# Optimization experiments

Hardware: AMD Instinct MI355X
Metric: run time of the kernel (lower is better)

The kernel has to match this reference:

```python
import jax, jax.numpy as jnp
import numpy as np

NUM_STEPS = 5  # matches init num_steps
N_NODES = 500_000
N_EDGES = 32_000_000


def setup_inputs() -> dict:
    key = jax.random.key(0)
    k1, k2, k3 = jax.random.split(key, 3)
    prior_probs = jax.random.uniform(k1, (N_NODES,), dtype=jnp.float32)
    edge_index = jax.random.randint(k2, (2, N_EDGES), 0, N_NODES, dtype=jnp.int32)
    edge_probs = jax.random.uniform(k3, (N_EDGES,), dtype=jnp.float32)
    return {"prior_probs": prior_probs, "edge_index": edge_index, "edge_probs": edge_probs}


def reference(prior_probs, edge_index, edge_probs):
    num_nodes = prior_probs.shape[0]
    source = edge_index[0]
    target = edge_index[1]
    p_t_u = prior_probs
    prod_terms = jnp.ones_like(prior_probs)
    for _ in range(NUM_STEPS):
        # gather node activation at source, weight by edge prob, scatter-add into target
        message = edge_probs * p_t_u[source]            # [E]
        agg = jax.ops.segment_sum(message, target, num_segments=num_nodes)  # [N]
        delta = 1.0 - jnp.exp(-agg)
        new_p_t_u = prod_terms * delta
        prod_terms = prod_terms * (1.0 - new_p_t_u)
        p_t_u = new_p_t_u
    p_final = 1.0 - prod_terms + prior_probs
    return p_final.reshape(-1, 1)
```

## Files before the change

### kernel.cpp

```cpp
#include <hip/hip_runtime.h>
#include <hip/hip_fp16.h>

#define NUM_STEPS 5
typedef unsigned int u32;

#define RSH 10
#define RSZ 1024
#define SB  512
#define HT  512
#define ST  512
#define NBMAX 512
#define BINS 8
#define SPLIT 2
#define SRC_BITS 19
#define SRC_MASK 0x7FFFFu

static inline size_t align256(size_t x){ return (x + 255) & ~(size_t)255; }


__global__ void init_fast(const float* __restrict__ prior, __half* __restrict__ p,
                          float* __restrict__ prod, int n){
    int i = blockIdx.x*blockDim.x + threadIdx.x;
    if(i<n){ p[i]=__float2half_rn(prior[i]); prod[i]=1.0f; }
}

__global__ void hist_kernel(const int* __restrict__ dst, long long E, int B,
                            u32* __restrict__ blk_cnt){
    extern __shared__ u32 hist[];
    int sb = blockIdx.x;
    long long E4 = E >> 2;
    long long chunk = (E4 + SB - 1)/SB;
    long long i0 = (long long)sb*chunk;
    long long i1 = i0 + chunk; if(i1 > E4) i1 = E4;
    for(int b=threadIdx.x; b<B; b+=blockDim.x) hist[b]=0;
    __syncthreads();
    const int4* d4 = (const int4*)dst;
    for(long long i=i0+threadIdx.x; i<i1; i+=blockDim.x){
        int4 d = d4[i];
        atomicAdd(&hist[((u32)d.x)>>RSH], 1u);
        atomicAdd(&hist[((u32)d.y)>>RSH], 1u);
        atomicAdd(&hist[((u32)d.z)>>RSH], 1u);
        atomicAdd(&hist[((u32)d.w)>>RSH], 1u);
    }
    if(sb==0){
        for(long long e=(E4<<2)+threadIdx.x; e<E; e+=blockDim.x)
            atomicAdd(&hist[((u32)dst[e])>>RSH], 1u);
    }
    __syncthreads();
    for(int b=threadIdx.x; b<B; b+=blockDim.x) blk_cnt[(size_t)sb*B + b] = hist[b];
}

__global__ void colscan_kernel(u32* __restrict__ blk_cnt, int B, u32* __restrict__ tot){
    __shared__ u32 s[SB];
    int b = blockIdx.x, t = threadIdx.x;
    u32 v = blk_cnt[(size_t)t*B + b];
    s[t] = v; __syncthreads();
    for(int off=1; off<SB; off<<=1){
        u32 x = (t>=off) ? s[t-off] : 0;
        __syncthreads();
        s[t] += x;
        __syncthreads();
    }
    blk_cnt[(size_t)t*B + b] = s[t] - v;
    if(t==SB-1) tot[b] = s[SB-1];
}

__global__ void basescan_kernel(const u32* __restrict__ tot, u32* __restrict__ base, int B){
    __shared__ u32 s[256];
    int t = threadIdx.x;
    u32 v0 = (2*t   < B) ? tot[2*t]   : 0;
    u32 v1 = (2*t+1 < B) ? tot[2*t+1] : 0;
    u32 sum = v0 + v1;
    s[t] = sum; __syncthreads();
    for(int off=1; off<256; off<<=1){
        u32 x = (t>=off) ? s[t-off] : 0;
        __syncthreads();
        s[t] += x;
        __syncthreads();
    }
    u32 run = s[t] - sum;
    if(2*t   < B) base[2*t]   = run;
    if(2*t+1 < B) base[2*t+1] = run + v0;
    if(t==255) base[B] = s[255];
}

__global__ __launch_bounds__(ST) void
scatter_kernel(const int* __restrict__ src, const int* __restrict__ dst,
               const float* __restrict__ ep, long long E, int B,
               const u32* __restrict__ blk_rel, const u32* __restrict__ base,
               uint2* __restrict__ edges){
    __shared__ uint2 bin[NBMAX][BINS];
    __shared__ u32 cnt[NBMAX];
    __shared__ u32 gcur[NBMAX];
    const int sb = blockIdx.x, t = threadIdx.x;
    long long E4 = E >> 2;
    long long chunk = (E4 + SB - 1)/SB;
    long long i0 = (long long)sb*chunk;
    long long i1 = i0 + chunk; if(i1 > E4) i1 = E4;
    for(int b=t; b<B; b+=ST){ cnt[b]=0; gcur[b]=base[b]+blk_rel[(size_t)sb*B+b]; }
    __syncthreads();
    const int4*   s4=(const int4*)src;
    const int4*   d4=(const int4*)dst;
    const float4* w4=(const float4*)ep;
    for(long long it=i0; it<i1; it+=ST){
        long long i = it + t;
        bool valid = (i < i1);
        u32 bk[4]; u32 sl[4]; uint2 pl[4];
        if(valid){
            int4 s=s4[i]; int4 d=d4[i]; float4 w=w4[i];
            u32 dd;
            dd=(u32)d.x; bk[0]=dd>>RSH; pl[0]=make_uint2(((u32)s.x)|((dd&(RSZ-1))<<SRC_BITS), __float_as_uint(w.x));
            dd=(u32)d.y; bk[1]=dd>>RSH; pl[1]=make_uint2(((u32)s.y)|((dd&(RSZ-1))<<SRC_BITS), __float_as_uint(w.y));
            dd=(u32)d.z; bk[2]=dd>>RSH; pl[2]=make_uint2(((u32)s.z)|((dd&(RSZ-1))<<SRC_BITS), __float_as_uint(w.z));
            dd=(u32)d.w; bk[3]=dd>>RSH; pl[3]=make_uint2(((u32)s.w)|((dd&(RSZ-1))<<SRC_BITS), __float_as_uint(w.w));
            #pragma unroll
            for(int k=0;k<4;k++) sl[k]=atomicAdd(&cnt[bk[k]],1u);
        }
        __syncthreads();
        if(valid){
            #pragma unroll
            for(int k=0;k<4;k++){
                if(sl[k] < BINS) bin[bk[k]][sl[k]] = pl[k];
                else             edges[gcur[bk[k]] + sl[k]] = pl[k];
            }
        }
        __syncthreads();
        for(int b=t; b<B; b+=ST){
            u32 c = cnt[b];
            if(c >= BINS){
                u32 g = gcur[b];
                #pragma unroll
                for(int k2=0;k2<BINS;k2++) edges[g+k2] = bin[b][k2];
                gcur[b] = g + c;
                cnt[b]  = 0;
            }
        }
        __syncthreads();
    }
    if(sb==0){
        long long tb = E4<<2;
        int nt = (int)(E - tb);
        if(nt > 0){
            bool v = (t < nt);
            u32 bk0=0, sl0=0; uint2 pl0=make_uint2(0,0);
            if(v){
                u32 dd=(u32)dst[tb+t]; bk0=dd>>RSH;
                pl0=make_uint2(((u32)src[tb+t])|((dd&(RSZ-1))<<SRC_BITS), __float_as_uint(ep[tb+t]));
                sl0=atomicAdd(&cnt[bk0],1u);
            }
            __syncthreads();
            if(v){ if(sl0<BINS) bin[bk0][sl0]=pl0; else edges[gcur[bk0]+sl0]=pl0; }
            __syncthreads();
        }
    }
    for(int b=t; b<B; b+=ST){
        u32 c = cnt[b]; if(c > BINS) c = BINS;
        u32 g = gcur[b];
        for(u32 k2=0;k2<c;k2++) edges[g+k2] = bin[b][k2];
    }
}

__global__ __launch_bounds__(512) void
step_kernel(const uint2* __restrict__ edges, const u32* __restrict__ base,
            const __half* __restrict__ p, float* __restrict__ pacc){
    __shared__ float acc[2][RSZ];
    int blk = blockIdx.x;
    int b   = blk >> 1;
    int part= blk & 1;
    int t   = threadIdx.x;
    for(int k=t; k<RSZ; k+=512){ acc[0][k]=0.0f; acc[1][k]=0.0f; }
    __syncthreads();
    u32 e0 = base[b], e1 = base[b+1];
    u32 cnt = e1 - e0;
    u32 s0 = e0 + (cnt*(u32)part)/SPLIT;
    u32 s1 = e0 + (cnt*(u32)(part+1))/SPLIT;
    int rep = t & 1;
    u32 n = s1 - s0;
    u32 m = n >> 11;
    u32 eb = s0 + t;
    for(u32 it=0; it<m; ++it){
        uint2 a0 = edges[eb];
        uint2 a1 = edges[eb+512];
        uint2 a2 = edges[eb+1024];
        uint2 a3 = edges[eb+1536];
        float p0 = __half2float(p[a0.x & SRC_MASK]);
        float p1 = __half2float(p[a1.x & SRC_MASK]);
        float p2 = __half2float(p[a2.x & SRC_MASK]);
        float p3 = __half2float(p[a3.x & SRC_MASK]);
        atomicAdd(&acc[rep][a0.x >> SRC_BITS], __uint_as_float(a0.y)*p0);
        atomicAdd(&acc[rep][a1.x >> SRC_BITS], __uint_as_float(a1.y)*p1);
        atomicAdd(&acc[rep][a2.x >> SRC_BITS], __uint_as_float(a2.y)*p2);
        atomicAdd(&acc[rep][a3.x >> SRC_BITS], __uint_as_float(a3.y)*p3);
        eb += 2048;
    }
    for(u32 e=eb; e<s1; e+=512){
        uint2 a = edges[e];
        atomicAdd(&acc[rep][a.x >> SRC_BITS],
                  __uint_as_float(a.y)*__half2float(p[a.x & SRC_MASK]));
    }
    __syncthreads();
    float* dstp = pacc + (size_t)blk * RSZ;
    for(int k=t; k<RSZ; k+=512) dstp[k] = acc[0][k] + acc[1][k];
}

__global__ void combine_kernel(const float* __restrict__ pacc, __half* __restrict__ p,
                               float* __restrict__ prod, const float* __restrict__ prior,
                               float* __restrict__ out, int n, int final_step){
    int i = blockIdx.x*blockDim.x + threadIdx.x;
    if(i < n){
        int b = i >> RSH, k = i & (RSZ-1);
        float a = pacc[(size_t)(b*SPLIT    )*RSZ + k]
                + pacc[(size_t)(b*SPLIT + 1)*RSZ + k];
        float pr_old = prod[i];
        float np = pr_old * (1.0f - expf(-a));
        float pr = pr_old * (1.0f - np);
        prod[i] = pr;
        p[i] = __float2half_rn(np);
        if(final_step) out[i] = 1.0f - pr + prior[i];
    }
}


__global__ void init_kernel(const float* __restrict__ prior, float* __restrict__ p,
                            float* __restrict__ prod, float* __restrict__ agg, int n){
    int i = blockIdx.x*blockDim.x + threadIdx.x;
    if(i<n){ p[i]=prior[i]; prod[i]=1.0f; agg[i]=0.0f; }
}

__global__ void edge_kernel(const int* __restrict__ src, const int* __restrict__ dst,
                            const float* __restrict__ ep, const float* __restrict__ p,
                            float* __restrict__ agg, int e4, int e_rem, long long e4base){
    int i = blockIdx.x*blockDim.x + threadIdx.x;
    if(i < e4){
        int4   s = ((const int4*)src)[i];
        int4   t = ((const int4*)dst)[i];
        float4 w = ((const float4*)ep)[i];
        atomicAdd(&agg[t.x], w.x * p[s.x]);
        atomicAdd(&agg[t.y], w.y * p[s.y]);
        atomicAdd(&agg[t.z], w.z * p[s.z]);
        atomicAdd(&agg[t.w], w.w * p[s.w]);
    }
    if(blockIdx.x==0 && threadIdx.x < e_rem){
        long long e = e4base + threadIdx.x;
        atomicAdd(&agg[dst[e]], ep[e]*p[src[e]]);
    }
}

__global__ void node_kernel(float* __restrict__ p, float* __restrict__ prod,
                            float* __restrict__ agg, const float* __restrict__ prior,
                            float* __restrict__ out, int n, int final_step){
    int i = blockIdx.x*blockDim.x + threadIdx.x;
    if(i<n){
        float a = agg[i]; agg[i]=0.0f;
        float pr_old = prod[i];
        float np = pr_old*(1.0f - expf(-a));
        float pr = pr_old*(1.0f - np);
        prod[i]=pr; p[i]=np;
        if(final_step) out[i] = 1.0f - pr + prior[i];
    }
}


extern "C" void kernel_launch(void* const* d_in, const int* in_sizes, int n_in,
                              void* d_out, int out_size, void* d_ws, size_t ws_size,
                              hipStream_t stream){
    const float* prior = (const float*)d_in[0];
    const int*   eidx  = (const int*)d_in[1];
    const float* ep    = (const float*)d_in[2];

    const int n = in_sizes[0];
    const long long E = (long long)in_sizes[2];
    const int* src = eidx;
    const int* dst = eidx + E;
    float* out = (float*)d_out;

    const int B = (n + RSZ - 1) >> RSH;

    size_t szNh  = align256((size_t)n * 2);
    size_t szN   = align256((size_t)n * 4);
    size_t szB1  = align256((size_t)(B + 1) * 4);
    size_t szB   = align256((size_t)B * 4);
    size_t szCnt = align256((size_t)SB * B * 4);
    size_t szAcc = align256((size_t)SPLIT * B * RSZ * 4);
    size_t szE2  = align256((size_t)E * 8);

    size_t off_p    = 0;
    size_t off_prod = off_p + szNh;
    size_t off_base = off_prod + szN;
    size_t off_tot  = off_base + szB1;
    size_t off_cnt  = off_tot + szB;
    size_t off_acc  = off_cnt + szCnt;
    size_t off_edge = off_acc + szAcc;
    size_t need     = off_edge + szE2;

    char* ws = (char*)d_ws;

    if(ws_size >= need && n < (1 << SRC_BITS) && B <= NBMAX){
        __half* p    = (__half*)(ws + off_p);
        float*  prod = (float*) (ws + off_prod);
        u32*    base = (u32*)   (ws + off_base);
        u32*    tot  = (u32*)   (ws + off_tot);
        u32*    cnt  = (u32*)   (ws + off_cnt);
        float*  pacc = (float*) (ws + off_acc);
        uint2*  edges= (uint2*) (ws + off_edge);

        const int nb_n = (n + 255)/256;
        init_fast<<<nb_n, 256, 0, stream>>>(prior, p, prod, n);
        hist_kernel<<<SB, HT, (size_t)B*4, stream>>>(dst, E, B, cnt);
        colscan_kernel<<<B, SB, 0, stream>>>(cnt, B, tot);
        basescan_kernel<<<1, 256, 0, stream>>>(tot, base, B);
        scatter_kernel<<<SB, ST, 0, stream>>>(src, dst, ep, E, B, cnt, base, edges);

        for(int step=0; step<NUM_STEPS; ++step){
            step_kernel<<<B*SPLIT, 512, 0, stream>>>(edges, base, p, pacc);
            combine_kernel<<<nb_n, 256, 0, stream>>>(pacc, p, prod, prior, out, n,
                                                     step == NUM_STEPS-1 ? 1 : 0);
        }
    } else {
        float* p    = (float*)d_ws;
        float* prod = p + n;
        float* agg  = prod + n;
        const int nb_n = (n + 255)/256;
        init_kernel<<<nb_n, 256, 0, stream>>>(prior, p, prod, agg, n);
        const int e4 = (int)(E/4);
        const int e_rem = (int)(E%4);
        const long long e4base = (long long)e4*4;
        const int nb_e = (e4 + 255)/256;
        for(int step=0; step<NUM_STEPS; ++step){
            edge_kernel<<<nb_e, 256, 0, stream>>>(src, dst, ep, p, agg, e4, e_rem, e4base);
            node_kernel<<<nb_n, 256, 0, stream>>>(p, prod, agg, prior, out, n,
                                                  step == NUM_STEPS-1 ? 1 : 0);
        }
    }
}
```

Before: 1.162 ms.

## Sub-sort edges by source within each destination bucket for gather locality

Adds a per-bucket counting sort that reorders the packed edges by the high bits of the source index into a second edge buffer. The step kernel then reads the sorted buffer, so its gathers of p[source] touch nearby addresses, which should cut scattered memory traffic across the five steps. SB also doubles to 1024 histogram/scatter blocks, and colscan gets a matching launch bound. The cost is one extra pass over all edges and a second E-sized workspace buffer; when the workspace is too small, the sort is skipped.

New measurement: 1.601 ms. 1.38x slower.

```diff
diff --git a/kernel.cpp b/kernel.cpp
--- a/kernel.cpp
+++ b/kernel.cpp
@@ -6,7 +6,7 @@
 
 #define RSH 10
 #define RSZ 1024
-#define SB  512
+#define SB  1024
 #define HT  512
 #define ST  512
 #define NBMAX 512
@@ -14,6 +14,8 @@
 #define SPLIT 2
 #define SRC_BITS 19
 #define SRC_MASK 0x7FFFFu
+#define SBIN 256
+#define SBIN_SH 11
 
 static inline size_t align256(size_t x){ return (x + 255) & ~(size_t)255; }
 
@@ -50,7 +52,8 @@
     for(int b=threadIdx.x; b<B; b+=blockDim.x) blk_cnt[(size_t)sb*B + b] = hist[b];
 }
 
-__global__ void colscan_kernel(u32* __restrict__ blk_cnt, int B, u32* __restrict__ tot){
+__global__ __launch_bounds__(SB) void
+colscan_kernel(u32* __restrict__ blk_cnt, int B, u32* __restrict__ tot){
     __shared__ u32 s[SB];
     int b = blockIdx.x, t = threadIdx.x;
     u32 v = blk_cnt[(size_t)t*B + b];
@@ -157,6 +160,37 @@
         u32 c = cnt[b]; if(c > BINS) c = BINS;
         u32 g = gcur[b];
         for(u32 k2=0;k2<c;k2++) edges[g+k2] = bin[b][k2];
+    }
+}
+
+__global__ __launch_bounds__(512) void
+srcsort_kernel(const uint2* __restrict__ in, const u32* __restrict__ base,
+               uint2* __restrict__ outb){
+    __shared__ u32 hist[SBIN];
+    __shared__ u32 scn[SBIN];
+    __shared__ u32 cur[SBIN];
+    int b = blockIdx.x, t = threadIdx.x;
+    u32 e0 = base[b], e1 = base[b+1];
+    if(t < SBIN) hist[t] = 0;
+    __syncthreads();
+    for(u32 e=e0+t; e<e1; e+=512)
+        atomicAdd(&hist[(in[e].x & SRC_MASK) >> SBIN_SH], 1u);
+    __syncthreads();
+    if(t < SBIN) scn[t] = hist[t];
+    __syncthreads();
+    for(int off=1; off<SBIN; off<<=1){
+        u32 x = 0;
+        if(t < SBIN && t >= off) x = scn[t-off];
+        __syncthreads();
+        if(t < SBIN) scn[t] += x;
+        __syncthreads();
+    }
+    if(t < SBIN) cur[t] = e0 + scn[t] - hist[t];
+    __syncthreads();
+    for(u32 e=e0+t; e<e1; e+=512){
+        uint2 pk = in[e];
+        u32 pos = atomicAdd(&cur[(pk.x & SRC_MASK) >> SBIN_SH], 1u);
+        outb[pos] = pk;
     }
 }
 
@@ -291,11 +325,13 @@
     size_t off_cnt  = off_tot + szB;
     size_t off_acc  = off_cnt + szCnt;
     size_t off_edge = off_acc + szAcc;
-    size_t need     = off_edge + szE2;
+    size_t need_ns  = off_edge + szE2;
+    size_t off_edg2 = need_ns;
+    size_t need_full= off_edg2 + szE2;
 
     char* ws = (char*)d_ws;
 
-    if(ws_size >= need && n < (1 << SRC_BITS) && B <= NBMAX){
+    if(ws_size >= need_ns && n < (1 << SRC_BITS) && B <= NBMAX){
         __half* p    = (__half*)(ws + off_p);
         float*  prod = (float*) (ws + off_prod);
         u32*    base = (u32*)   (ws + off_base);
@@ -303,6 +339,8 @@
         u32*    cnt  = (u32*)   (ws + off_cnt);
         float*  pacc = (float*) (ws + off_acc);
         uint2*  edges= (uint2*) (ws + off_edge);
+        uint2*  edg2 = (uint2*) (ws + off_edg2);
+        const bool do_sort = (ws_size >= need_full);
 
         const int nb_n = (n + 255)/256;
         init_fast<<<nb_n, 256, 0, stream>>>(prior, p, prod, n);
@@ -311,8 +349,14 @@
         basescan_kernel<<<1, 256, 0, stream>>>(tot, base, B);
         scatter_kernel<<<SB, ST, 0, stream>>>(src, dst, ep, E, B, cnt, base, edges);
 
+        const uint2* step_edges = edges;
+        if(do_sort){
+            srcsort_kernel<<<B, 512, 0, stream>>>(edges, base, edg2);
+            step_edges = edg2;
+        }
+
         for(int step=0; step<NUM_STEPS; ++step){
-            step_kernel<<<B*SPLIT, 512, 0, stream>>>(edges, base, p, pacc);
+            step_kernel<<<B*SPLIT, 512, 0, stream>>>(step_edges, base, p, pacc);
             combine_kernel<<<nb_n, 256, 0, stream>>>(pacc, p, prod, prior, out, n,
                                                      step == NUM_STEPS-1 ? 1 : 0);
         }
```

## Fuse all propagation steps into one cooperative kernel with grid sync

Applied to the files above, without the earlier changes.

Replaces the per-step step_kernel plus combine_kernel pairs, and the init kernel, with a single cooperative launch. Each block owns one 1024-node bucket, keeps the node's product term in a register and accumulates in shared memory, and uses grid.sync between phases. This removes the global partial-accumulator round trip and repeated launches, but loses the SPLIT=2 edge partitioning and the 4-way unrolled loads. The histogram scatter block count (SB) is also doubled. It relies on all B (~489) blocks of 1024 threads being co-resident for cooperative launch.

Result: slower. 3.599 ms (+209.7%).

```diff
diff --git a/kernel.cpp b/kernel.cpp
--- a/kernel.cpp
+++ b/kernel.cpp
@@ -1,28 +1,24 @@
 #include <hip/hip_runtime.h>
 #include <hip/hip_fp16.h>
+#include <hip/hip_cooperative_groups.h>
+
+namespace cg = cooperative_groups;
 
 #define NUM_STEPS 5
 typedef unsigned int u32;
 
 #define RSH 10
 #define RSZ 1024
-#define SB  512
+#define SB  1024
 #define HT  512
 #define ST  512
 #define NBMAX 512
 #define BINS 8
-#define SPLIT 2
 #define SRC_BITS 19
 #define SRC_MASK 0x7FFFFu
 
 static inline size_t align256(size_t x){ return (x + 255) & ~(size_t)255; }
 
-
-__global__ void init_fast(const float* __restrict__ prior, __half* __restrict__ p,
-                          float* __restrict__ prod, int n){
-    int i = blockIdx.x*blockDim.x + threadIdx.x;
-    if(i<n){ p[i]=__float2half_rn(prior[i]); prod[i]=1.0f; }
-}
 
 __global__ void hist_kernel(const int* __restrict__ dst, long long E, int B,
                             u32* __restrict__ blk_cnt){
@@ -50,7 +46,8 @@
     for(int b=threadIdx.x; b<B; b+=blockDim.x) blk_cnt[(size_t)sb*B + b] = hist[b];
 }
 
-__global__ void colscan_kernel(u32* __restrict__ blk_cnt, int B, u32* __restrict__ tot){
+__global__ __launch_bounds__(SB) void
+colscan_kernel(u32* __restrict__ blk_cnt, int B, u32* __restrict__ tot){
     __shared__ u32 s[SB];
     int b = blockIdx.x, t = threadIdx.x;
     u32 v = blk_cnt[(size_t)t*B + b];
@@ -160,64 +157,38 @@
     }
 }
 
-__global__ __launch_bounds__(512) void
-step_kernel(const uint2* __restrict__ edges, const u32* __restrict__ base,
-            const __half* __restrict__ p, float* __restrict__ pacc){
+__global__ __launch_bounds__(1024, 2) void
+fused_steps(const uint2* __restrict__ edges, const u32* __restrict__ base,
+            __half* __restrict__ p, const float* __restrict__ prior,
+            float* __restrict__ out, int n){
+    cg::grid_group grid = cg::this_grid();
     __shared__ float acc[2][RSZ];
-    int blk = blockIdx.x;
-    int b   = blk >> 1;
-    int part= blk & 1;
-    int t   = threadIdx.x;
-    for(int k=t; k<RSZ; k+=512){ acc[0][k]=0.0f; acc[1][k]=0.0f; }
-    __syncthreads();
-    u32 e0 = base[b], e1 = base[b+1];
-    u32 cnt = e1 - e0;
-    u32 s0 = e0 + (cnt*(u32)part)/SPLIT;
-    u32 s1 = e0 + (cnt*(u32)(part+1))/SPLIT;
-    int rep = t & 1;
-    u32 n = s1 - s0;
-    u32 m = n >> 11;
-    u32 eb = s0 + t;
-    for(u32 it=0; it<m; ++it){
-        uint2 a0 = edges[eb];
-        uint2 a1 = edges[eb+512];
-        uint2 a2 = edges[eb+1024];
-        uint2 a3 = edges[eb+1536];
-        float p0 = __half2float(p[a0.x & SRC_MASK]);
-        float p1 = __half2float(p[a1.x & SRC_MASK]);
-        float p2 = __half2float(p[a2.x & SRC_MASK]);
-        float p3 = __half2float(p[a3.x & SRC_MASK]);
-        atomicAdd(&acc[rep][a0.x >> SRC_BITS], __uint_as_float(a0.y)*p0);
-        atomicAdd(&acc[rep][a1.x >> SRC_BITS], __uint_as_float(a1.y)*p1);
-        atomicAdd(&acc[rep][a2.x >> SRC_BITS], __uint_as_float(a2.y)*p2);
-        atomicAdd(&acc[rep][a3.x >> SRC_BITS], __uint_as_float(a3.y)*p3);
-        eb += 2048;
-    }
-    for(u32 e=eb; e<s1; e+=512){
-        uint2 a = edges[e];
-        atomicAdd(&acc[rep][a.x >> SRC_BITS],
-                  __uint_as_float(a.y)*__half2float(p[a.x & SRC_MASK]));
-    }
-    __syncthreads();
-    float* dstp = pacc + (size_t)blk * RSZ;
-    for(int k=t; k<RSZ; k+=512) dstp[k] = acc[0][k] + acc[1][k];
-}
-
-__global__ void combine_kernel(const float* __restrict__ pacc, __half* __restrict__ p,
-                               float* __restrict__ prod, const float* __restrict__ prior,
-                               float* __restrict__ out, int n, int final_step){
-    int i = blockIdx.x*blockDim.x + threadIdx.x;
-    if(i < n){
-        int b = i >> RSH, k = i & (RSZ-1);
-        float a = pacc[(size_t)(b*SPLIT    )*RSZ + k]
-                + pacc[(size_t)(b*SPLIT + 1)*RSZ + k];
-        float pr_old = prod[i];
-        float np = pr_old * (1.0f - expf(-a));
-        float pr = pr_old * (1.0f - np);
-        prod[i] = pr;
-        p[i] = __float2half_rn(np);
-        if(final_step) out[i] = 1.0f - pr + prior[i];
-    }
+    const int b = blockIdx.x, t = threadIdx.x;
+    const int i = (b << RSH) + t;
+    acc[0][t] = 0.0f; acc[1][t] = 0.0f;
+    if(i < n) p[i] = __float2half_rn(prior[i]);
+    float prodr = 1.0f;
+    const u32 e0 = base[b], e1 = base[b+1];
+    const int rep = t & 1;
+    __threadfence();
+    grid.sync();
+    for(int step=0; step<NUM_STEPS; ++step){
+        for(u32 e = e0 + t; e < e1; e += 1024){
+            uint2 pk = edges[e];
+            atomicAdd(&acc[rep][pk.x >> SRC_BITS],
+                      __uint_as_float(pk.y) * __half2float(p[pk.x & SRC_MASK]));
+        }
+        __threadfence();
+        grid.sync();
+        float a = acc[0][t] + acc[1][t];
+        acc[0][t] = 0.0f; acc[1][t] = 0.0f;
+        float np = prodr * (1.0f - expf(-a));
+        prodr *= (1.0f - np);
+        if(i < n) p[i] = __float2half_rn(np);
+        __threadfence();
+        grid.sync();
+    }
+    if(i < n) out[i] = 1.0f - prodr + prior[i];
 }
 
 
@@ -277,45 +248,37 @@
     const int B = (n + RSZ - 1) >> RSH;
 
     size_t szNh  = align256((size_t)n * 2);
-    size_t szN   = align256((size_t)n * 4);
     size_t szB1  = align256((size_t)(B + 1) * 4);
     size_t szB   = align256((size_t)B * 4);
     size_t szCnt = align256((size_t)SB * B * 4);
-    size_t szAcc = align256((size_t)SPLIT * B * RSZ * 4);
     size_t szE2  = align256((size_t)E * 8);
 
     size_t off_p    = 0;
-    size_t off_prod = off_p + szNh;
-    size_t off_base = off_prod + szN;
+    size_t off_base = off_p + szNh;
     size_t off_tot  = off_base + szB1;
     size_t off_cnt  = off_tot + szB;
-    size_t off_acc  = off_cnt + szCnt;
-    size_t off_edge = off_acc + szAcc;
+    size_t off_edge = off_cnt + szCnt;
     size_t need     = off_edge + szE2;
 
     char* ws = (char*)d_ws;
 
     if(ws_size >= need && n < (1 << SRC_BITS) && B <= NBMAX){
         __half* p    = (__half*)(ws + off_p);
-        float*  prod = (float*) (ws + off_prod);
         u32*    base = (u32*)   (ws + off_base);
         u32*    tot  = (u32*)   (ws + off_tot);
         u32*    cnt  = (u32*)   (ws + off_cnt);
-        float*  pacc = (float*) (ws + off_acc);
         uint2*  edges= (uint2*) (ws + off_edge);
 
-        const int nb_n = (n + 255)/256;
-        init_fast<<<nb_n, 256, 0, stream>>>(prior, p, prod, n);
         hist_kernel<<<SB, HT, (size_t)B*4, stream>>>(dst, E, B, cnt);
         colscan_kernel<<<B, SB, 0, stream>>>(cnt, B, tot);
         basescan_kernel<<<1, 256, 0, stream>>>(tot, base, B);
         scatter_kernel<<<SB, ST, 0, stream>>>(src, dst, ep, E, B, cnt, base, edges);
 
-        for(int step=0; step<NUM_STEPS; ++step){
-            step_kernel<<<B*SPLIT, 512, 0, stream>>>(edges, base, p, pacc);
-            combine_kernel<<<nb_n, 256, 0, stream>>>(pacc, p, prod, prior, out, n,
-                                                     step == NUM_STEPS-1 ? 1 : 0);
-        }
+        int n_arg = n;
+        void* args[] = { (void*)&edges, (void*)&base, (void*)&p,
+                         (void*)&prior, (void*)&out, (void*)&n_arg };
+        hipLaunchCooperativeKernel((const void*)fused_steps,
+                                   dim3(B), dim3(1024), args, 0, stream);
     } else {
         float* p    = (float*)d_ws;
         float* prod = p + n;
```
